# Optimization experiments

Hardware: AMD Instinct MI355X
Metric: run time of the kernel (lower is better)

The kernel has to match this reference:

```python
import jax, jax.numpy as jnp
import numpy as np

B, S, D, H = 4, 2048, 1024, 16
HD = D // H  # head dim = 64


def setup_inputs() -> dict:
    key = jax.random.key(0)
    ks = jax.random.split(key, 5)
    scale = 1.0 / np.sqrt(D)
    return {
        "X": jax.random.normal(ks[0], (B, S, D), dtype=jnp.float32),
        "Wq": jax.random.normal(ks[1], (D, D), dtype=jnp.float32) * scale,
        "Wk": jax.random.normal(ks[2], (D, D), dtype=jnp.float32) * scale,
        "Wv": jax.random.normal(ks[3], (D, D), dtype=jnp.float32) * scale,
        "Wo": jax.random.normal(ks[4], (D, D), dtype=jnp.float32) * scale,
    }


def _split_heads(x):
    # [B, S, D] -> [B, H, S, HD]
    b, s, d = x.shape
    return x.reshape(b, s, H, HD).transpose(0, 2, 1, 3)


def reference(X, Wq, Wk, Wv, Wo):
    q = _split_heads(X @ Wq)  # [B, H, S, HD]
    k = _split_heads(X @ Wk)
    v = _split_heads(X @ Wv)
    scores = jnp.einsum("bhqd,bhkd->bhqk", q, k) / jnp.sqrt(jnp.float32(HD))
    causal = jnp.tril(jnp.ones((S, S), dtype=bool))  # [S, S]
    scores = jnp.where(causal[None, None, :, :], scores, jnp.float32(-jnp.inf))
    attn = jax.nn.softmax(scores, axis=-1)
    out = jnp.einsum("bhqk,bhkd->bhqd", attn, v)  # [B, H, S, HD]
    out = out.transpose(0, 2, 1, 3).reshape(B, S, D)  # merge heads
    return out @ Wo
```

## Files before the change

### kernel.cpp

```cpp
#include <hip/hip_runtime.h>
#include <hip/hip_bf16.h>

typedef __attribute__((ext_vector_type(8))) short short8;
typedef __attribute__((ext_vector_type(8))) unsigned short ushort8;
typedef __attribute__((ext_vector_type(4))) unsigned short bf16x4;
typedef __attribute__((ext_vector_type(4))) float f32x4;

#define BDIM 1024
#define SEQ  2048
#define NHD  16
#define NEGBIG (-1.0e30f)

__device__ __forceinline__ unsigned short f2bf(float x) {
  union { __hip_bfloat16 h; unsigned short u; } cv;
  cv.h = __float2bfloat16(x);
  return cv.u;
}

__device__ __forceinline__ void gload16(const void* g, void* l) {
  __builtin_amdgcn_global_load_lds((const __attribute__((address_space(1))) void*)g,
                                   (__attribute__((address_space(3))) void*)l, 16, 0, 0);
}

__global__ __launch_bounds__(256) void prep(const float* __restrict__ X, unsigned short* __restrict__ Xb,
                                            const float* __restrict__ s0, const float* __restrict__ s1,
                                            const float* __restrict__ s2, const float* __restrict__ s3,
                                            unsigned short* __restrict__ d0, unsigned short* __restrict__ d1,
                                            unsigned short* __restrict__ d2, unsigned short* __restrict__ d3) {
  const int z = blockIdx.z;
  const int tid = threadIdx.y * 32 + threadIdx.x;
  if (z >= 4) {
    int i = (((z - 4) * 1024 + blockIdx.y * 32 + blockIdx.x) * 256 + tid) * 8;
    float4 a = *(const float4*)(X + i);
    float4 b = *(const float4*)(X + i + 4);
    ushort8 o;
    o[0] = f2bf(a.x); o[1] = f2bf(a.y); o[2] = f2bf(a.z); o[3] = f2bf(a.w);
    o[4] = f2bf(b.x); o[5] = f2bf(b.y); o[6] = f2bf(b.z); o[7] = f2bf(b.w);
    *(ushort8*)(Xb + i) = o;
    return;
  }
  const float* src = z == 0 ? s0 : z == 1 ? s1 : z == 2 ? s2 : s3;
  unsigned short* dst = z == 0 ? d0 : z == 1 ? d1 : z == 2 ? d2 : d3;
  __shared__ float t[32][33];
  int tx = threadIdx.x, ty = threadIdx.y;
  int c0 = blockIdx.x * 32, r0 = blockIdx.y * 32;
  for (int i = ty; i < 32; i += 8)
    t[i][tx] = src[(size_t)(r0 + i) * BDIM + c0 + tx];
  __syncthreads();
  for (int i = ty; i < 32; i += 8)
    dst[(size_t)(c0 + i) * BDIM + r0 + tx] = f2bf(t[tx][i]);
}

template <bool F32OUT>
__device__ __forceinline__ void gemm_body(const unsigned short* __restrict__ A,
                                          const unsigned short* __restrict__ BT,
                                          void* __restrict__ Cv,
                                          unsigned short* As, unsigned short* Bs) {
  const int tid = threadIdx.x;
  const int lane = tid & 63;
  const int w = tid >> 6;
  const int wr = w >> 1, wc = w & 1;
  const int m0 = blockIdx.x * 128;
  const int n0 = blockIdx.y * 128;
  const int l15 = lane & 15, lg = lane >> 4;

  int ob[4], grow[4], gcol[4];
  for (int j = 0; j < 4; ++j) {
    ob[j] = (w * 4 + j) * 1024;
    int o = ob[j] + lane * 16;
    int row = o >> 7;
    int kb = (o & 127) ^ ((row & 7) << 4);
    grow[j] = row; gcol[j] = kb >> 1;
  }

  f32x4 acc[4][4] = {};

  for (int j = 0; j < 4; ++j) {
    gload16(A + (size_t)(m0 + grow[j]) * BDIM + gcol[j], (char*)As + ob[j]);
    gload16(BT + (size_t)(n0 + grow[j]) * BDIM + gcol[j], (char*)Bs + ob[j]);
  }
  __syncthreads();

  int cur = 0;
  for (int k0 = 0; k0 < BDIM; k0 += 64) {
    if (k0 + 64 < BDIM) {
      int nb = (cur ^ 1) * 16384;
      for (int j = 0; j < 4; ++j) {
        gload16(A + (size_t)(m0 + grow[j]) * BDIM + (k0 + 64) + gcol[j], (char*)As + nb + ob[j]);
        gload16(BT + (size_t)(n0 + grow[j]) * BDIM + (k0 + 64) + gcol[j], (char*)Bs + nb + ob[j]);
      }
    }
    const char* Ab = (const char*)As + cur * 16384;
    const char* Bb = (const char*)Bs + cur * 16384;
    for (int ks = 0; ks < 64; ks += 32) {
      int kb = (ks + lg * 8) * 2;
      short8 a[4], b[4];
      for (int mi = 0; mi < 4; ++mi) {
        int row = wr * 64 + mi * 16 + l15;
        a[mi] = *(const short8*)(Ab + row * 128 + (kb ^ ((row & 7) << 4)));
      }
      for (int nj = 0; nj < 4; ++nj) {
        int row = wc * 64 + nj * 16 + l15;
        b[nj] = *(const short8*)(Bb + row * 128 + (kb ^ ((row & 7) << 4)));
      }
      for (int mi = 0; mi < 4; ++mi)
        for (int nj = 0; nj < 4; ++nj)
          acc[mi][nj] = __builtin_amdgcn_mfma_f32_16x16x32_bf16(a[mi], b[nj], acc[mi][nj], 0, 0, 0);
    }
    __syncthreads();
    cur ^= 1;
  }

  for (int mi = 0; mi < 4; ++mi)
    for (int nj = 0; nj < 4; ++nj) {
      int m = m0 + wr * 64 + mi * 16 + lg * 4;
      int n = n0 + wc * 64 + nj * 16 + l15;
      for (int r = 0; r < 4; ++r) {
        if constexpr (F32OUT)
          ((float*)Cv)[(size_t)(m + r) * BDIM + n] = acc[mi][nj][r];
        else
          ((unsigned short*)Cv)[(size_t)(m + r) * BDIM + n] = f2bf(acc[mi][nj][r]);
      }
    }
}

__global__ __launch_bounds__(256) void gemm_qkv(const unsigned short* __restrict__ A,
                                                const unsigned short* __restrict__ B0,
                                                const unsigned short* __restrict__ B1,
                                                const unsigned short* __restrict__ B2,
                                                unsigned short* __restrict__ C0,
                                                unsigned short* __restrict__ C1,
                                                unsigned short* __restrict__ C2) {
  __shared__ __align__(16) unsigned short As[2 * 128 * 64];
  __shared__ __align__(16) unsigned short Bs[2 * 128 * 64];
  const unsigned short* BT = blockIdx.z == 0 ? B0 : blockIdx.z == 1 ? B1 : B2;
  unsigned short* C = blockIdx.z == 0 ? C0 : blockIdx.z == 1 ? C1 : C2;
  gemm_body<false>(A, BT, C, As, Bs);
}

template <bool F32OUT>
__global__ __launch_bounds__(256) void gemm_bt(const unsigned short* __restrict__ A,
                                               const unsigned short* __restrict__ BT,
                                               void* __restrict__ Cv) {
  __shared__ __align__(16) unsigned short As[2 * 128 * 64];
  __shared__ __align__(16) unsigned short Bs[2 * 128 * 64];
  gemm_body<F32OUT>(A, BT, Cv, As, Bs);
}

__global__ __launch_bounds__(256) void attn(const unsigned short* __restrict__ Qg,
                                            const unsigned short* __restrict__ Kg,
                                            const unsigned short* __restrict__ Vg,
                                            unsigned short* __restrict__ Og) {
  __shared__ __align__(16) unsigned short Ks[64 * 64];
  __shared__ __align__(16) unsigned short VTs[64 * 64];
  __shared__ __align__(16) unsigned short Ps[128 * 64];

  const int tid = threadIdx.x;
  const int lane = tid & 63;
  const int w = tid >> 6;
  const int l15 = lane & 15, lg = lane >> 4;
  const int bh = blockIdx.x;
  const size_t base = ((size_t)(bh >> 4) * SEQ) * BDIM + (size_t)(bh & 15) * 64;
  constexpr float C = 0.125f * 1.44269504089f;
  constexpr float MB = 96.0f * C;

  const int srow = tid >> 3;
  const int scol = (((tid & 7) * 16) ^ ((srow & 7) << 4)) >> 1;
  const int sdst = tid * 16;
  const int vp = tid & 31, vd = tid >> 5;
  int vdst[8];
  for (int e = 0; e < 8; ++e) {
    int d = vd * 8 + e;
    vdst[e] = d * 128 + ((4 * vp) ^ ((((d & 7) ^ (d >> 3)) & 7) << 4));
  }

  const int by = blockIdx.y;
  const int g = by >> 2, j = by & 3;
  const int c = g == 0 ? 15 - 2 * j : g == 1 ? 2 * j : g == 2 ? 14 - 2 * j : 1 + 2 * j;
  const int q0 = c * 128;

  for (int p = 0; p < 4; ++p)
    gload16(Qg + base + (size_t)(q0 + p * 32 + srow) * BDIM + scol, (char*)Ps + p * 4096 + sdst);
  __syncthreads();
  short8 qf[2][2];
  for (int mi = 0; mi < 2; ++mi) {
    int row = w * 32 + mi * 16 + l15;
    int sz = (row & 7) << 4;
    qf[mi][0] = *(const short8*)((const char*)Ps + row * 128 + ((lg * 16) ^ sz));
    qf[mi][1] = *(const short8*)((const char*)Ps + row * 128 + ((64 + lg * 16) ^ sz));
  }

  float lrow[2] = {0.f, 0.f};
  f32x4 oacc[2][4] = {};

  const int ntiles = 2 * c + 2;

  ushort8 v0, v1;
  gload16(Kg + base + (size_t)(srow) * BDIM + scol, (char*)Ks + sdst);
  gload16(Kg + base + (size_t)(32 + srow) * BDIM + scol, (char*)Ks + 4096 + sdst);
  {
    const unsigned short* vs = Vg + base + (size_t)(2 * vp) * BDIM + vd * 8;
    v0 = *(const ushort8*)vs;
    v1 = *(const ushort8*)(vs + BDIM);
  }
  for (int e = 0; e < 8; ++e) {
    unsigned int pk = (unsigned int)v0[e] | ((unsigned int)v1[e] << 16);
    *(unsigned int*)((char*)VTs + vdst[e]) = pk;
  }
  __syncthreads();

  for (int t = 0; t < ntiles; ++t) {
    const int kv0 = t * 64;
    const bool more = (t + 1 < ntiles);
    const bool live = kv0 <= q0 + w * 32 + 31;

    if (more) {
      const unsigned short* vs = Vg + base + (size_t)(kv0 + 64 + 2 * vp) * BDIM + vd * 8;
      v0 = *(const ushort8*)vs;
      v1 = *(const ushort8*)(vs + BDIM);
    }

    f32x4 s2[2][4];
    if (live) {
      __builtin_amdgcn_s_setprio(1);
      for (int kvj = 0; kvj < 4; ++kvj) {
        int row = kvj * 16 + l15;
        int sz = (row & 7) << 4;
        short8 kf0 = *(const short8*)((const char*)Ks + row * 128 + ((lg * 16) ^ sz));
        short8 kf1 = *(const short8*)((const char*)Ks + row * 128 + ((64 + lg * 16) ^ sz));
        for (int mi = 0; mi < 2; ++mi) {
          f32x4 z = {};
          z = __builtin_amdgcn_mfma_f32_16x16x32_bf16(kf0, qf[mi][0], z, 0, 0, 0);
          z = __builtin_amdgcn_mfma_f32_16x16x32_bf16(kf1, qf[mi][1], z, 0, 0, 0);
          s2[mi][kvj] = z;
        }
      }
      __builtin_amdgcn_s_setprio(0);
    }
    __syncthreads();

    if (more) {
      gload16(Kg + base + (size_t)(kv0 + 64 + srow) * BDIM + scol, (char*)Ks + sdst);
      gload16(Kg + base + (size_t)(kv0 + 96 + srow) * BDIM + scol, (char*)Ks + 4096 + sdst);
    }

    if (live) {
      for (int mi = 0; mi < 2; ++mi) {
        const int qbase = q0 + w * 32 + mi * 16;
        if (kv0 > qbase + 15) {
          continue;
        }
        const int qc = qbase + l15;
        if (kv0 + 63 > qbase) {
          for (int kvj = 0; kvj < 4; ++kvj)
            for (int r = 0; r < 4; ++r) {
              int kv = kv0 + kvj * 16 + 4 * lg + r;
              if (kv > qc) s2[mi][kvj][r] = NEGBIG;
            }
        }
        float ps[4];
        for (int kvj = 0; kvj < 4; ++kvj) {
          float p0 = __builtin_amdgcn_exp2f(fmaf(s2[mi][kvj][0], C, -MB));
          float p1 = __builtin_amdgcn_exp2f(fmaf(s2[mi][kvj][1], C, -MB));
          float p2 = __builtin_amdgcn_exp2f(fmaf(s2[mi][kvj][2], C, -MB));
          float p3 = __builtin_amdgcn_exp2f(fmaf(s2[mi][kvj][3], C, -MB));
          s2[mi][kvj][0] = p0; s2[mi][kvj][1] = p1; s2[mi][kvj][2] = p2; s2[mi][kvj][3] = p3;
          ps[kvj] = (p0 + p1) + (p2 + p3);
        }
        float rs = (ps[0] + ps[1]) + (ps[2] + ps[3]);
        rs += __shfl_xor(rs, 16);
        rs += __shfl_xor(rs, 32);
        lrow[mi] += rs;
        int prow = w * 32 + mi * 16 + l15;
        int psz = (prow & 7) << 4;
        for (int kvj = 0; kvj < 4; ++kvj) {
          bf16x4 pk;
          pk[0] = f2bf(s2[mi][kvj][0]); pk[1] = f2bf(s2[mi][kvj][1]);
          pk[2] = f2bf(s2[mi][kvj][2]); pk[3] = f2bf(s2[mi][kvj][3]);
          *(bf16x4*)((char*)Ps + prow * 128 + ((kvj * 32 + lg * 8) ^ psz)) = pk;
        }
      }
      __builtin_amdgcn_s_setprio(1);
      for (int ks = 0; ks < 2; ++ks) {
        short8 pa[2], vf[4];
        for (int mi = 0; mi < 2; ++mi) {
          int prow = w * 32 + mi * 16 + l15;
          pa[mi] = *(const short8*)((const char*)Ps + prow * 128 +
                                    ((ks * 64 + lg * 16) ^ ((prow & 7) << 4)));
        }
        for (int di = 0; di < 4; ++di) {
          int d = di * 16 + l15;
          vf[di] = *(const short8*)((const char*)VTs + d * 128 +
                                    ((ks * 64 + lg * 16) ^ ((((d & 7) ^ (d >> 3)) & 7) << 4)));
        }
        for (int mi = 0; mi < 2; ++mi)
          for (int di = 0; di < 4; ++di)
            oacc[mi][di] = __builtin_amdgcn_mfma_f32_16x16x32_bf16(vf[di], pa[mi], oacc[mi][di], 0, 0, 0);
      }
      __builtin_amdgcn_s_setprio(0);
    }
    __syncthreads();

    if (more) {
      for (int e = 0; e < 8; ++e) {
        unsigned int pk = (unsigned int)v0[e] | ((unsigned int)v1[e] << 16);
        *(unsigned int*)((char*)VTs + vdst[e]) = pk;
      }
    }
  }

  for (int mi = 0; mi < 2; ++mi) {
    float inv = 1.0f / lrow[mi];
    int qrow = q0 + w * 32 + mi * 16 + l15;
    for (int di = 0; di < 4; ++di) {
      bf16x4 ov;
      for (int r = 0; r < 4; ++r) ov[r] = f2bf(oacc[mi][di][r] * inv);
      *(bf16x4*)(Og + base + (size_t)qrow * BDIM + di * 16 + 4 * lg) = ov;
    }
  }
}

extern "C" void kernel_launch(void* const* d_in, const int* in_sizes, int n_in,
                              void* d_out, int out_size, void* d_ws, size_t ws_size,
                              hipStream_t stream) {
  const float* X  = (const float*)d_in[0];
  const float* Wq = (const float*)d_in[1];
  const float* Wk = (const float*)d_in[2];
  const float* Wv = (const float*)d_in[3];
  const float* Wo = (const float*)d_in[4];

  const size_t WSZ = (size_t)1024 * 1024;
  const size_t MSZ = (size_t)8192 * 1024;
  const size_t need = (4 * WSZ + 4 * MSZ) * 2;
  if (ws_size < need) return;

  unsigned short* ws = (unsigned short*)d_ws;
  unsigned short* WqT = ws;
  unsigned short* WkT = WqT + WSZ;
  unsigned short* WvT = WkT + WSZ;
  unsigned short* WoT = WvT + WSZ;
  unsigned short* Qw  = WoT + WSZ;
  unsigned short* Kw  = Qw + MSZ;
  unsigned short* Vw  = Kw + MSZ;
  unsigned short* Ow  = Vw + MSZ;
  unsigned short* Xb  = (unsigned short*)d_out;

  prep<<<dim3(32, 32, 8), dim3(32, 8), 0, stream>>>(X, Xb, Wq, Wk, Wv, Wo, WqT, WkT, WvT, WoT);

  gemm_qkv<<<dim3(64, 8, 3), 256, 0, stream>>>(Xb, WqT, WkT, WvT, Qw, Kw, Vw);

  attn<<<dim3(64, 16), 256, 0, stream>>>(Qw, Kw, Vw, Ow);

  gemm_bt<true><<<dim3(64, 8), 256, 0, stream>>>(Ow, WoT, d_out);
}
```

Before: 168.4 us.

## Double-buffer K/V tiles in attention and enlarge query block to 256 rows

The attention kernel now uses 512 threads covering 256 query rows per block, with a 64-row tile per wave group, and halves the grid along the query dimension. K and V^T tiles are double-buffered in shared memory, so the next tile's loads are issued before the current tile's compute and one barrier per iteration is removed. This aims to overlap global loads with MFMA work and to reuse each K/V tile across more query rows. In exchange it uses more LDS per block and fewer blocks, and the causal imbalance between blocks grows with the coarser query tiles.

```diff
diff --git a/kernel.cpp b/kernel.cpp
--- a/kernel.cpp
+++ b/kernel.cpp
@@ -147,13 +147,13 @@
   gemm_body<F32OUT>(A, BT, Cv, As, Bs);
 }
 
-__global__ __launch_bounds__(256) void attn(const unsigned short* __restrict__ Qg,
+__global__ __launch_bounds__(512) void attn(const unsigned short* __restrict__ Qg,
                                             const unsigned short* __restrict__ Kg,
                                             const unsigned short* __restrict__ Vg,
                                             unsigned short* __restrict__ Og) {
-  __shared__ __align__(16) unsigned short Ks[64 * 64];
-  __shared__ __align__(16) unsigned short VTs[64 * 64];
-  __shared__ __align__(16) unsigned short Ps[128 * 64];
+  __shared__ __align__(16) unsigned short Ks[2][64 * 64];
+  __shared__ __align__(16) unsigned short VTs[2][64 * 64];
+  __shared__ __align__(16) unsigned short Ps[256 * 64];
 
   const int tid = threadIdx.x;
   const int lane = tid & 63;
@@ -168,19 +168,18 @@
   const int scol = (((tid & 7) * 16) ^ ((srow & 7) << 4)) >> 1;
   const int sdst = tid * 16;
   const int vp = tid & 31, vd = tid >> 5;
-  int vdst[8];
-  for (int e = 0; e < 8; ++e) {
-    int d = vd * 8 + e;
+  int vdst[4];
+  for (int e = 0; e < 4; ++e) {
+    int d = vd * 4 + e;
     vdst[e] = d * 128 + ((4 * vp) ^ ((((d & 7) ^ (d >> 3)) & 7) << 4));
   }
 
   const int by = blockIdx.y;
-  const int g = by >> 2, j = by & 3;
-  const int c = g == 0 ? 15 - 2 * j : g == 1 ? 2 * j : g == 2 ? 14 - 2 * j : 1 + 2 * j;
-  const int q0 = c * 128;
+  const int c = by < 4 ? 7 - by : by - 4;
+  const int q0 = c * 256;
 
   for (int p = 0; p < 4; ++p)
-    gload16(Qg + base + (size_t)(q0 + p * 32 + srow) * BDIM + scol, (char*)Ps + p * 4096 + sdst);
+    gload16(Qg + base + (size_t)(q0 + p * 64 + srow) * BDIM + scol, (char*)Ps + p * 8192 + sdst);
   __syncthreads();
   short8 qf[2][2];
   for (int mi = 0; mi < 2; ++mi) {
@@ -193,41 +192,43 @@
   float lrow[2] = {0.f, 0.f};
   f32x4 oacc[2][4] = {};
 
-  const int ntiles = 2 * c + 2;
-
-  ushort8 v0, v1;
-  gload16(Kg + base + (size_t)(srow) * BDIM + scol, (char*)Ks + sdst);
-  gload16(Kg + base + (size_t)(32 + srow) * BDIM + scol, (char*)Ks + 4096 + sdst);
+  const int ntiles = 4 * c + 4;
+
+  bf16x4 v0, v1;
+  gload16(Kg + base + (size_t)(srow) * BDIM + scol, (char*)Ks[0] + sdst);
   {
-    const unsigned short* vs = Vg + base + (size_t)(2 * vp) * BDIM + vd * 8;
-    v0 = *(const ushort8*)vs;
-    v1 = *(const ushort8*)(vs + BDIM);
-  }
-  for (int e = 0; e < 8; ++e) {
+    const unsigned short* vs = Vg + base + (size_t)(2 * vp) * BDIM + vd * 4;
+    v0 = *(const bf16x4*)vs;
+    v1 = *(const bf16x4*)(vs + BDIM);
+  }
+  for (int e = 0; e < 4; ++e) {
     unsigned int pk = (unsigned int)v0[e] | ((unsigned int)v1[e] << 16);
-    *(unsigned int*)((char*)VTs + vdst[e]) = pk;
+    *(unsigned int*)((char*)VTs[0] + vdst[e]) = pk;
   }
   __syncthreads();
 
+  int cur = 0;
   for (int t = 0; t < ntiles; ++t) {
     const int kv0 = t * 64;
     const bool more = (t + 1 < ntiles);
     const bool live = kv0 <= q0 + w * 32 + 31;
 
     if (more) {
-      const unsigned short* vs = Vg + base + (size_t)(kv0 + 64 + 2 * vp) * BDIM + vd * 8;
-      v0 = *(const ushort8*)vs;
-      v1 = *(const ushort8*)(vs + BDIM);
-    }
-
-    f32x4 s2[2][4];
+      const int nv0 = kv0 + 64;
+      gload16(Kg + base + (size_t)(nv0 + srow) * BDIM + scol, (char*)Ks[cur ^ 1] + sdst);
+      const unsigned short* vs = Vg + base + (size_t)(nv0 + 2 * vp) * BDIM + vd * 4;
+      v0 = *(const bf16x4*)vs;
+      v1 = *(const bf16x4*)(vs + BDIM);
+    }
+
     if (live) {
+      f32x4 s2[2][4];
       __builtin_amdgcn_s_setprio(1);
       for (int kvj = 0; kvj < 4; ++kvj) {
         int row = kvj * 16 + l15;
         int sz = (row & 7) << 4;
-        short8 kf0 = *(const short8*)((const char*)Ks + row * 128 + ((lg * 16) ^ sz));
-        short8 kf1 = *(const short8*)((const char*)Ks + row * 128 + ((64 + lg * 16) ^ sz));
+        short8 kf0 = *(const short8*)((const char*)Ks[cur] + row * 128 + ((lg * 16) ^ sz));
+        short8 kf1 = *(const short8*)((const char*)Ks[cur] + row * 128 + ((64 + lg * 16) ^ sz));
         for (int mi = 0; mi < 2; ++mi) {
           f32x4 z = {};
           z = __builtin_amdgcn_mfma_f32_16x16x32_bf16(kf0, qf[mi][0], z, 0, 0, 0);
@@ -236,20 +237,10 @@
         }
       }
       __builtin_amdgcn_s_setprio(0);
-    }
-    __syncthreads();
-
-    if (more) {
-      gload16(Kg + base + (size_t)(kv0 + 64 + srow) * BDIM + scol, (char*)Ks + sdst);
-      gload16(Kg + base + (size_t)(kv0 + 96 + srow) * BDIM + scol, (char*)Ks + 4096 + sdst);
-    }
-
-    if (live) {
+
       for (int mi = 0; mi < 2; ++mi) {
         const int qbase = q0 + w * 32 + mi * 16;
-        if (kv0 > qbase + 15) {
-          continue;
-        }
+        if (kv0 > qbase + 15) continue;
         const int qc = qbase + l15;
         if (kv0 + 63 > qbase) {
           for (int kvj = 0; kvj < 4; ++kvj)
@@ -290,7 +281,7 @@
         }
         for (int di = 0; di < 4; ++di) {
           int d = di * 16 + l15;
-          vf[di] = *(const short8*)((const char*)VTs + d * 128 +
+          vf[di] = *(const short8*)((const char*)VTs[cur] + d * 128 +
                                     ((ks * 64 + lg * 16) ^ ((((d & 7) ^ (d >> 3)) & 7) << 4)));
         }
         for (int mi = 0; mi < 2; ++mi)
@@ -299,14 +290,15 @@
       }
       __builtin_amdgcn_s_setprio(0);
     }
+
+    if (more) {
+      for (int e = 0; e < 4; ++e) {
+        unsigned int pk = (unsigned int)v0[e] | ((unsigned int)v1[e] << 16);
+        *(unsigned int*)((char*)VTs[cur ^ 1] + vdst[e]) = pk;
+      }
+    }
     __syncthreads();
-
-    if (more) {
-      for (int e = 0; e < 8; ++e) {
-        unsigned int pk = (unsigned int)v0[e] | ((unsigned int)v1[e] << 16);
-        *(unsigned int*)((char*)VTs + vdst[e]) = pk;
-      }
-    }
+    cur ^= 1;
   }
 
   for (int mi = 0; mi < 2; ++mi) {
@@ -349,7 +341,7 @@
 
   gemm_qkv<<<dim3(64, 8, 3), 256, 0, stream>>>(Xb, WqT, WkT, WvT, Qw, Kw, Vw);
 
-  attn<<<dim3(64, 16), 256, 0, stream>>>(Qw, Kw, Vw, Ow);
+  attn<<<dim3(64, 8), 512, 0, stream>>>(Qw, Kw, Vw, Ow);
 
   gemm_bt<true><<<dim3(64, 8), 256, 0, stream>>>(Ow, WoT, d_out);
 }
```

Measured after the change: 169.4 us. About the same (+0.6%).
